# Performance work log

Measured on AMD Instinct MI355X. Metric: run time of the kernel, lower is better.

The kernel has to match this reference:

```python
import jax, jax.numpy as jnp
import numpy as np

DIM = 512
NUM_HEADS = 8
HEAD_DIM = DIM // NUM_HEADS
EPS = 1e-6


def setup_inputs() -> dict:
    key = jax.random.key(0)
    k_x, k_qkv, k_out, k_b = jax.random.split(key, 4)
    B, N = 8, 4096
    x = jax.random.normal(k_x, (B, N, DIM), dtype=jnp.float32)
    # nn.Linear weights stored as [out_features, in_features]; we keep [in, out] for x @ W
    s_qkv = 1.0 / np.sqrt(DIM)
    W_qkv = jax.random.uniform(k_qkv, (DIM, 3 * DIM), minval=-s_qkv, maxval=s_qkv, dtype=jnp.float32)
    W_out = jax.random.uniform(k_out, (DIM, DIM), minval=-s_qkv, maxval=s_qkv, dtype=jnp.float32)
    b_out = jax.random.uniform(k_b, (DIM,), minval=-s_qkv, maxval=s_qkv, dtype=jnp.float32)
    return {"x": x, "W_qkv": W_qkv, "W_out": W_out, "b_out": b_out}


def _feature_map(x):
    # elu(x) + 1
    return jax.nn.elu(x) + 1.0


def reference(x, W_qkv, W_out, b_out):
    B, N, C = x.shape
    H, D = NUM_HEADS, HEAD_DIM
    qkv = x @ W_qkv                              # [B, N, 3C]
    qkv = qkv.reshape(B, N, 3, H, D).transpose(2, 0, 3, 1, 4)  # [3, B, H, N, D]
    q, k, v = qkv[0], qkv[1], qkv[2]
    q_phi = _feature_map(q)                      # [B, H, N, D]
    k_phi = _feature_map(k)
    KV = jnp.einsum('bhnd,bhne->bhde', k_phi, v)  # [B, H, D, D]
    K_sum = k_phi.sum(axis=2)                     # [B, H, D]
    denom = jnp.einsum('bhnd,bhd->bhn', q_phi, K_sum)[..., None] + EPS  # [B, H, N, 1]
    out = jnp.einsum('bhnd,bhde->bhne', q_phi, KV) / denom              # [B, H, N, D]
    out = out.transpose(0, 2, 1, 3).reshape(B, N, C)
    return out @ W_out + b_out
```

## Files before the change

### kernel.cpp

```cpp
#include <hip/hip_runtime.h>
#include <stdint.h>

typedef float    f32x4 __attribute__((ext_vector_type(4)));
typedef short    s16x8 __attribute__((ext_vector_type(8)));
typedef short    s16x4 __attribute__((ext_vector_type(4)));
typedef unsigned short u16;
typedef uint32_t u32;

#define DEVINL __device__ __forceinline__

DEVINL float bf2f(u16 u) { union { u32 i; float f; } x; x.i = ((u32)u) << 16; return x.f; }
DEVINL u16 f2bf(float f) {
  union { float f; u32 i; } x; x.f = f;
  u32 i = x.i;
  return (u16)((i + 0x7FFFu + ((i >> 16) & 1u)) >> 16);
}

DEVINL void gload16(const void* g, void* l) {
  __builtin_amdgcn_global_load_lds((const __attribute__((address_space(1))) void*)g,
                                   (__attribute__((address_space(3))) void*)l,
                                   16, 0, 0);
}

__global__ __launch_bounds__(256) void k_prep(const float* __restrict__ x,
                                              u16* __restrict__ xb,
                                              const float* __restrict__ Wqkv,
                                              u16* __restrict__ wqkvt,
                                              const float* __restrict__ Wout,
                                              u16* __restrict__ woutt) {
  __shared__ __align__(16) float t[64][65];
  int b = blockIdx.x;
  int tid = threadIdx.x;
  if (b < 2048) {
    const int n8 = 2097152;
    int stride = 2048 * 256;
    for (int i = b * 256 + tid; i < n8; i += stride) {
      const f32x4* p = (const f32x4*)(x + (size_t)i * 8);
      f32x4 a = p[0], c = p[1];
      s16x8 o;
      o[0] = (short)f2bf(a[0]); o[1] = (short)f2bf(a[1]);
      o[2] = (short)f2bf(a[2]); o[3] = (short)f2bf(a[3]);
      o[4] = (short)f2bf(c[0]); o[5] = (short)f2bf(c[1]);
      o[6] = (short)f2bf(c[2]); o[7] = (short)f2bf(c[3]);
      *(s16x8*)(xb + (size_t)i * 8) = o;
    }
    return;
  }
  const float* W; u16* Wt; int K, N, tb;
  if (b < 2048 + 192) { W = Wqkv; Wt = wqkvt; K = 512; N = 1536; tb = b - 2048; }
  else               { W = Wout; Wt = woutt; K = 512; N = 512;  tb = b - 2240; }
  int nb = N >> 6;
  int tn = tb % nb, tk = tb / nb;
  int n0 = tn << 6, k0 = tk << 6;
  int cr = tid >> 4, cc = (tid & 15) << 2;
#pragma unroll
  for (int i = 0; i < 4; i++) {
    int r = cr + (i << 4);
    f32x4 v = *(const f32x4*)(W + (size_t)(k0 + r) * N + n0 + cc);
    t[r][cc] = v[0]; t[r][cc + 1] = v[1]; t[r][cc + 2] = v[2]; t[r][cc + 3] = v[3];
  }
  __syncthreads();
#pragma unroll
  for (int i = 0; i < 4; i++) {
    int nn = cr + (i << 4);
    s16x4 o;
    o[0] = (short)f2bf(t[cc    ][nn]);
    o[1] = (short)f2bf(t[cc + 1][nn]);
    o[2] = (short)f2bf(t[cc + 2][nn]);
    o[3] = (short)f2bf(t[cc + 3][nn]);
    *(s16x4*)(Wt + (size_t)(n0 + nn) * K + k0 + cc) = o;
  }
}

template <int EPI>
__global__ __launch_bounds__(512, 1) void k_gemm(
    const u16* __restrict__ A, const u16* __restrict__ Bt,
    int nbn,
    u16* __restrict__ qph, u16* __restrict__ kphT, u16* __restrict__ vT,
    float* __restrict__ out, const float* __restrict__ bias) {
  __shared__ __align__(16) u16 lsA[3][256 * 32];
  __shared__ __align__(16) u16 lsB[3][256 * 32];

  int nwg = gridDim.x;
  int bx = blockIdx.x;
  int o = (bx & 7) * (nwg >> 3) + (bx >> 3);
  int bm = o / nbn, bn = o % nbn;
  int m0 = bm << 8, n0 = bn << 8;
  int tid = threadIdx.x;
  int w = tid >> 6, lane = tid & 63;
  int lnlo = lane & 15, lnhi = lane >> 4;
  int wr = w >> 2, wc = w & 3;

  const u16* gAp[2]; const u16* gBp[2]; int ldst[2];
#pragma unroll
  for (int i = 0; i < 2; i++) {
    int c = tid + i * 512;
    int row = c >> 2, ch = c & 3;
    int gch = ch ^ ((row >> 1) & 3);
    gAp[i] = A + (size_t)(m0 + row) * 512 + gch * 8;
    gBp[i] = Bt + (size_t)(n0 + row) * 512 + gch * 8;
    ldst[i] = c * 8;
  }

  int offA[8], offB[4];
#pragma unroll
  for (int f = 0; f < 8; f++) {
    int r = wr * 128 + f * 16 + lnlo;
    offA[f] = r * 32 + (lnhi ^ ((r >> 1) & 3)) * 8;
  }
#pragma unroll
  for (int f = 0; f < 4; f++) {
    int r = wc * 64 + f * 16 + lnlo;
    offB[f] = r * 32 + (lnhi ^ ((r >> 1) & 3)) * 8;
  }

  f32x4 acc[8][4] = {};

#pragma unroll
  for (int i = 0; i < 2; i++) gload16(gAp[i], &lsA[0][ldst[i]]);
#pragma unroll
  for (int i = 0; i < 2; i++) gload16(gBp[i], &lsB[0][ldst[i]]);
#pragma unroll
  for (int i = 0; i < 2; i++) gload16(gAp[i] + 32, &lsA[1][ldst[i]]);
#pragma unroll
  for (int i = 0; i < 2; i++) gload16(gBp[i] + 32, &lsB[1][ldst[i]]);
  asm volatile("s_waitcnt vmcnt(4)" ::: "memory");
  __builtin_amdgcn_s_barrier();

#pragma unroll
  for (int t = 0; t < 16; t++) {
    int buf = t % 3;
    const u16* La = &lsA[buf][0];
    const u16* Lb = &lsB[buf][0];
    int k2 = (t + 2) * 32;
    int b2 = (t + 2) % 3;

    s16x8 bf[4], af[4];
#pragma unroll
    for (int f = 0; f < 4; f++) bf[f] = *(const s16x8*)(Lb + offB[f]);
#pragma unroll
    for (int f = 0; f < 4; f++) af[f] = *(const s16x8*)(La + offA[f]);
    if (t < 14) {
#pragma unroll
      for (int i = 0; i < 2; i++) gload16(gAp[i] + k2, &lsA[b2][ldst[i]]);
    }
    __builtin_amdgcn_s_barrier();
    __builtin_amdgcn_s_setprio(1);
#pragma unroll
    for (int mf = 0; mf < 4; mf++)
#pragma unroll
      for (int nf = 0; nf < 4; nf++)
        acc[mf][nf] = __builtin_amdgcn_mfma_f32_16x16x32_bf16(af[mf], bf[nf], acc[mf][nf], 0, 0, 0);
    __builtin_amdgcn_s_setprio(0);
    __builtin_amdgcn_s_barrier();

    s16x8 af2[4];
#pragma unroll
    for (int f = 0; f < 4; f++) af2[f] = *(const s16x8*)(La + offA[4 + f]);
    if (t < 14) {
#pragma unroll
      for (int i = 0; i < 2; i++) gload16(gBp[i] + k2, &lsB[b2][ldst[i]]);
    }
    __builtin_amdgcn_s_barrier();
    __builtin_amdgcn_s_setprio(1);
#pragma unroll
    for (int mf = 0; mf < 4; mf++)
#pragma unroll
      for (int nf = 0; nf < 4; nf++)
        acc[4 + mf][nf] = __builtin_amdgcn_mfma_f32_16x16x32_bf16(af2[mf], bf[nf], acc[4 + mf][nf], 0, 0, 0);
    __builtin_amdgcn_s_setprio(0);
    if (t <= 13)      asm volatile("s_waitcnt vmcnt(4)" ::: "memory");
    else if (t == 14) asm volatile("s_waitcnt vmcnt(0)" ::: "memory");
    if (t < 15) __builtin_amdgcn_s_barrier();
  }

  int gmB = m0 + wr * 128;
  int gnB = n0 + wc * 64;
  if (EPI == 0) {
    int sec = n0 >> 9;
    if (sec == 0) {
#pragma unroll
      for (int mf = 0; mf < 8; mf++) {
#pragma unroll
        for (int nf = 0; nf < 4; nf++) {
          int col = gnB + nf * 16 + lnlo;
          int hh = (col >> 6) & 7;
          int dd = col & 63;
#pragma unroll
          for (int r = 0; r < 4; r++) {
            int rowm = gmB + mf * 16 + lnhi * 4 + r;
            float val = acc[mf][nf][r];
            val = (val > 0.f) ? (val + 1.f) : __expf(val);
            int bidx = rowm >> 12, tok = rowm & 4095;
            qph[(((size_t)(bidx * 8 + hh) * 4096 + tok) << 6) + dd] = f2bf(val);
          }
        }
      }
    } else {
      u16* dstT = (sec == 1) ? kphT : vT;
      bool isphi = (sec == 1);
#pragma unroll
      for (int mf = 0; mf < 8; mf++) {
        int rowm = gmB + mf * 16 + lnhi * 4;
        int bidx = rowm >> 12, tok = rowm & 4095;
#pragma unroll
        for (int nf = 0; nf < 4; nf++) {
          int col = gnB + nf * 16 + lnlo;
          int hh = (col >> 6) & 7;
          int dd = col & 63;
          s16x4 o4;
#pragma unroll
          for (int r = 0; r < 4; r++) {
            float val = acc[mf][nf][r];
            if (isphi) val = (val > 0.f) ? (val + 1.f) : __expf(val);
            o4[r] = (short)f2bf(val);
          }
          *(s16x4*)&dstT[((size_t)(bidx * 8 + hh) * 64 + dd) * 4096 + tok] = o4;
        }
      }
    }
  } else {
#pragma unroll
    for (int mf = 0; mf < 8; mf++) {
#pragma unroll
      for (int nf = 0; nf < 4; nf++) {
        int col = gnB + nf * 16 + lnlo;
        float bv = bias[col];
#pragma unroll
        for (int r = 0; r < 4; r++) {
          int rowm = gmB + mf * 16 + lnhi * 4 + r;
          out[(size_t)rowm * 512 + col] = acc[mf][nf][r] + bv;
        }
      }
    }
  }
}

__global__ __launch_bounds__(256, 2) void k_kv(const u16* __restrict__ kphT,
                                               const u16* __restrict__ vT,
                                               float* __restrict__ kvpart,
                                               float* __restrict__ kspart) {
  __shared__ __align__(16) u16 lsK[64 * 256];
  __shared__ __align__(16) u16 lsV[64 * 256];
  __shared__ float red[4][64];
  int bx = blockIdx.x;
  int bh = bx >> 4, ck = bx & 15;
  int tid = threadIdx.x, w = tid >> 6, lane = tid & 63;
  int lnlo = lane & 15, lnhi = lane >> 4;
  size_t gbase = (size_t)bh * 64 * 4096 + ck * 256;

#pragma unroll
  for (int i = 0; i < 8; i++) {
    int c = tid + i * 256;
    int row = c >> 5, ch = c & 31;
    int gch = ch ^ (row & 31);
    gload16(kphT + gbase + (size_t)row * 4096 + gch * 8, &lsK[c * 8]);
  }
#pragma unroll
  for (int i = 0; i < 8; i++) {
    int c = tid + i * 256;
    int row = c >> 5, ch = c & 31;
    int gch = ch ^ (row & 31);
    gload16(vT + gbase + (size_t)row * 4096 + gch * 8, &lsV[c * 8]);
  }
  asm volatile("s_waitcnt vmcnt(0)" ::: "memory");
  __builtin_amdgcn_s_barrier();

  f32x4 acc[4] = {{0.f, 0.f, 0.f, 0.f}, {0.f, 0.f, 0.f, 0.f},
                  {0.f, 0.f, 0.f, 0.f}, {0.f, 0.f, 0.f, 0.f}};
  int rb = w * 16 + lnlo;
#pragma unroll
  for (int kk = 0; kk < 8; kk++) {
    s16x8 bfr = *(const s16x8*)&lsV[rb * 256 + ((kk * 4 + lnhi) ^ (rb & 31)) * 8];
#pragma unroll
    for (int mf = 0; mf < 4; mf++) {
      int ra = mf * 16 + lnlo;
      s16x8 af = *(const s16x8*)&lsK[ra * 256 + ((kk * 4 + lnhi) ^ (ra & 31)) * 8];
      acc[mf] = __builtin_amdgcn_mfma_f32_16x16x32_bf16(af, bfr, acc[mf], 0, 0, 0);
    }
  }

  {
    int d = tid & 63, q = tid >> 6;
    float s = 0.f;
#pragma unroll
    for (int j = 0; j < 8; j++) {
      s16x8 v8 = *(const s16x8*)&lsK[d * 256 + (q * 8 + j) * 8];
#pragma unroll
      for (int e = 0; e < 8; e++) s += bf2f((u16)v8[e]);
    }
    red[q][d] = s;
  }
  __syncthreads();

  size_t pb = (size_t)(bh * 16 + ck) * 4096;
#pragma unroll
  for (int mf = 0; mf < 4; mf++)
#pragma unroll
    for (int r = 0; r < 4; r++)
      kvpart[pb + (size_t)(mf * 16 + lnhi * 4 + r) * 64 + (w * 16 + lnlo)] = acc[mf][r];
  if (tid < 64)
    kspart[(size_t)(bh * 16 + ck) * 64 + tid] =
        red[0][tid] + red[1][tid] + red[2][tid] + red[3][tid];
}

__global__ __launch_bounds__(256) void k_kvred(const float* __restrict__ kvpart,
                                               const float* __restrict__ kspart,
                                               u16* __restrict__ kvt_sw,
                                               float* __restrict__ ksum) {
  int bh = blockIdx.x;
  int tid = threadIdx.x;
  int e = tid >> 2, d0 = (tid & 3) * 16;
  size_t pb = (size_t)bh * 16 * 4096;
#pragma unroll
  for (int dd = 0; dd < 16; dd++) {
    int d = d0 + dd;
    float s = 0.f;
#pragma unroll
    for (int c = 0; c < 16; c++) s += kvpart[pb + (size_t)c * 4096 + d * 64 + e];
    int chs = (d >> 3) ^ (e & 7);
    kvt_sw[((size_t)bh * 64 + e) * 64 + chs * 8 + (d & 7)] = f2bf(s);
  }
  if (tid < 64) {
    float s = 0.f;
#pragma unroll
    for (int c = 0; c < 16; c++) s += kspart[(size_t)bh * 1024 + c * 64 + tid];
    ksum[bh * 64 + tid] = s;
  }
}

__global__ __launch_bounds__(256, 2) void k_attnout(const u16* __restrict__ qphi,
                                                    const u16* __restrict__ kvt_sw,
                                                    const float* __restrict__ ksum,
                                                    u16* __restrict__ y) {
  __shared__ __align__(16) u16 qa[256 * 64];
  __shared__ __align__(16) u16 bb[64 * 64];
  __shared__ float ksl[64];
  __shared__ float rdnl[256];
  int bx = blockIdx.x;
  int bh = bx >> 4, tch = bx & 15;
  int b = bh >> 3, hh = bh & 7;
  int tid = threadIdx.x, w = tid >> 6, lane = tid & 63;
  int lnlo = lane & 15, lnhi = lane >> 4;
  size_t qbase = ((size_t)bh * 4096 + tch * 256) * 64;

#pragma unroll
  for (int i = 0; i < 8; i++) {
    int c = i * 256 + tid;
    int row = c >> 3, ch = c & 7;
    int gcol = (ch ^ (row & 7)) << 3;
    gload16(qphi + qbase + (size_t)row * 64 + gcol, &qa[c * 8]);
  }
#pragma unroll
  for (int i = 0; i < 2; i++) {
    int c = i * 256 + tid;
    gload16(kvt_sw + (size_t)bh * 4096 + c * 8, &bb[c * 8]);
  }
  if (tid < 64) ksl[tid] = ksum[bh * 64 + tid];
  __syncthreads();

  {
    float den = 0.f;
#pragma unroll
    for (int ch = 0; ch < 8; ch++) {
      s16x8 v8 = *(const s16x8*)&qa[tid * 64 + ((ch ^ (tid & 7)) << 3)];
#pragma unroll
      for (int j = 0; j < 8; j++) den += bf2f((u16)v8[j]) * ksl[ch * 8 + j];
    }
    rdnl[tid] = 1.f / (den + 1e-6f);
  }
  __syncthreads();

  f32x4 acc[4][4] = {};
#pragma unroll
  for (int kk = 0; kk < 2; kk++) {
    s16x8 af[4], bfr[4];
#pragma unroll
    for (int f = 0; f < 4; f++) {
      int ra = w * 64 + f * 16 + lnlo;
      int ca = (kk * 4 + lnhi) ^ (ra & 7);
      af[f] = *(const s16x8*)&qa[ra * 64 + ca * 8];
      int rb = f * 16 + lnlo;
      int cb = (kk * 4 + lnhi) ^ (rb & 7);
      bfr[f] = *(const s16x8*)&bb[rb * 64 + cb * 8];
    }
#pragma unroll
    for (int mf = 0; mf < 4; mf++)
#pragma unroll
      for (int nf = 0; nf < 4; nf++)
        acc[mf][nf] = __builtin_amdgcn_mfma_f32_16x16x32_bf16(af[mf], bfr[nf], acc[mf][nf], 0, 0, 0);
  }

  size_t yrow0 = (size_t)b * 4096 + tch * 256;
#pragma unroll
  for (int mf = 0; mf < 4; mf++) {
#pragma unroll
    for (int nf = 0; nf < 4; nf++) {
      int e = nf * 16 + lnlo;
#pragma unroll
      for (int r = 0; r < 4; r++) {
        int tl = w * 64 + mf * 16 + lnhi * 4 + r;
        float val = acc[mf][nf][r] * rdnl[tl];
        y[(yrow0 + tl) * 512 + hh * 64 + e] = f2bf(val);
      }
    }
  }
}

#define OFF_XB     ((size_t)0)
#define OFF_WQKVT  ((size_t)33554432)
#define OFF_WOUTT  ((size_t)35127296)
#define OFF_QPHI   ((size_t)35651584)
#define OFF_KPHI   ((size_t)69206016)
#define OFF_VBUF   ((size_t)102760448)
#define OFF_KVPART ((size_t)136314880)
#define OFF_KSPART ((size_t)153092096)
#define OFF_KVT    ((size_t)153354240)
#define OFF_KSUM   ((size_t)153878528)

extern "C" void kernel_launch(void* const* d_in, const int* in_sizes, int n_in,
                              void* d_out, int out_size, void* d_ws, size_t ws_size,
                              hipStream_t stream) {
  const float* x    = (const float*)d_in[0];
  const float* Wqkv = (const float*)d_in[1];
  const float* Wout = (const float*)d_in[2];
  const float* bout = (const float*)d_in[3];
  float* out = (float*)d_out;
  char* ws = (char*)d_ws;

  u16* xb     = (u16*)(ws + OFF_XB);
  u16* y      = (u16*)(ws + OFF_XB);
  u16* wqkvt  = (u16*)(ws + OFF_WQKVT);
  u16* woutt  = (u16*)(ws + OFF_WOUTT);
  u16* qphi   = (u16*)(ws + OFF_QPHI);
  u16* kphT   = (u16*)(ws + OFF_KPHI);
  u16* vT     = (u16*)(ws + OFF_VBUF);
  float* kvpart = (float*)(ws + OFF_KVPART);
  float* kspart = (float*)(ws + OFF_KSPART);
  u16* kvt_sw = (u16*)(ws + OFF_KVT);
  float* ksum = (float*)(ws + OFF_KSUM);

  k_prep<<<2304, 256, 0, stream>>>(x, xb, Wqkv, wqkvt, Wout, woutt);

  k_gemm<0><<<768, 512, 0, stream>>>(xb, wqkvt, 6, qphi, kphT, vT, nullptr, nullptr);
  k_kv<<<64 * 16, 256, 0, stream>>>(kphT, vT, kvpart, kspart);
  k_kvred<<<64, 256, 0, stream>>>(kvpart, kspart, kvt_sw, ksum);
  k_attnout<<<64 * 16, 256, 0, stream>>>(qphi, kvt_sw, ksum, y);
  k_gemm<1><<<256, 512, 0, stream>>>(y, woutt, 2, nullptr, nullptr, nullptr, out, bout);
}
```

Measured before the change: 159.3 us.

## Restructure GEMM main loop to double-buffered 64-wide K tiles with split half-tile loads

The GEMM mainloop moves from a triple-buffered 32-wide K tile to a double-buffered 64-wide K tile. Each operand buffer is split into two 128-row halves that are refilled at a finer grain, interleaved between MFMA groups, with an 8-way XOR swizzle on LDS. The goal is fewer barrier and loop iterations per K, and global-to-LDS loads that overlap more evenly with MFMA work. In exchange it adds many more barriers per tile and a hand-tuned vmcnt schedule that must match the issue order exactly.

```diff
diff --git a/kernel.cpp b/kernel.cpp
--- a/kernel.cpp
+++ b/kernel.cpp
@@ -8,6 +8,7 @@
 typedef uint32_t u32;
 
 #define DEVINL __device__ __forceinline__
+#define BARF do { asm volatile("" ::: "memory"); __builtin_amdgcn_s_barrier(); asm volatile("" ::: "memory"); } while (0)
 
 DEVINL float bf2f(u16 u) { union { u32 i; float f; } x; x.i = ((u32)u) << 16; return x.f; }
 DEVINL u16 f2bf(float f) {
@@ -74,104 +75,119 @@
 
 template <int EPI>
 __global__ __launch_bounds__(512, 1) void k_gemm(
-    const u16* __restrict__ A, const u16* __restrict__ Bt,
-    int nbn,
+    const u16* __restrict__ A, const u16* __restrict__ Bt, int nbn,
     u16* __restrict__ qph, u16* __restrict__ kphT, u16* __restrict__ vT,
     float* __restrict__ out, const float* __restrict__ bias) {
-  __shared__ __align__(16) u16 lsA[3][256 * 32];
-  __shared__ __align__(16) u16 lsB[3][256 * 32];
-
-  int nwg = gridDim.x;
-  int bx = blockIdx.x;
+  __shared__ __align__(16) u16 lsA[2][2][128 * 64];
+  __shared__ __align__(16) u16 lsB[2][2][128 * 64];
+
+  int nwg = gridDim.x, bx = blockIdx.x;
   int o = (bx & 7) * (nwg >> 3) + (bx >> 3);
   int bm = o / nbn, bn = o % nbn;
   int m0 = bm << 8, n0 = bn << 8;
-  int tid = threadIdx.x;
-  int w = tid >> 6, lane = tid & 63;
+  int tid = threadIdx.x, w = tid >> 6, lane = tid & 63;
   int lnlo = lane & 15, lnhi = lane >> 4;
   int wr = w >> 2, wc = w & 3;
 
-  const u16* gAp[2]; const u16* gBp[2]; int ldst[2];
-#pragma unroll
-  for (int i = 0; i < 2; i++) {
-    int c = tid + i * 512;
-    int row = c >> 2, ch = c & 3;
-    int gch = ch ^ ((row >> 1) & 3);
-    gAp[i] = A + (size_t)(m0 + row) * 512 + gch * 8;
-    gBp[i] = Bt + (size_t)(n0 + row) * 512 + gch * 8;
-    ldst[i] = c * 8;
-  }
-
-  int offA[8], offB[4];
-#pragma unroll
-  for (int f = 0; f < 8; f++) {
-    int r = wr * 128 + f * 16 + lnlo;
-    offA[f] = r * 32 + (lnhi ^ ((r >> 1) & 3)) * 8;
-  }
-#pragma unroll
-  for (int f = 0; f < 4; f++) {
-    int r = wc * 64 + f * 16 + lnlo;
-    offB[f] = r * 32 + (lnhi ^ ((r >> 1) & 3)) * 8;
-  }
+  int c0 = tid, c1 = tid + 512;
+  int r0 = c0 >> 3, r1 = c1 >> 3;
+  int g0 = ((c0 & 7) ^ (r0 & 7)) * 8, g1 = ((c1 & 7) ^ (r1 & 7)) * 8;
+  const u16* gA[2][2]; const u16* gB[2][2];
+#pragma unroll
+  for (int h = 0; h < 2; h++) {
+    gA[h][0] = A + (size_t)(m0 + h * 128 + r0) * 512 + g0;
+    gA[h][1] = A + (size_t)(m0 + h * 128 + r1) * 512 + g1;
+    gB[h][0] = Bt + (size_t)(n0 + h * 128 + r0) * 512 + g0;
+    gB[h][1] = Bt + (size_t)(n0 + h * 128 + r1) * 512 + g1;
+  }
+  int l0 = c0 * 8, l1 = c1 * 8;
+
+  auto SA = [&](int buf, int h, int kt) {
+    gload16(gA[h][0] + kt * 64, &lsA[buf][h][l0]);
+    gload16(gA[h][1] + kt * 64, &lsA[buf][h][l1]);
+  };
+  auto SB = [&](int buf, int h, int kt) {
+    gload16(gB[h][0] + kt * 64, &lsB[buf][h][l0]);
+    gload16(gB[h][1] + kt * 64, &lsB[buf][h][l1]);
+  };
+
+  int offA[2][8], offB[2][4];
+#pragma unroll
+  for (int kk = 0; kk < 2; kk++) {
+#pragma unroll
+    for (int mf = 0; mf < 8; mf++) {
+      int r = mf * 16 + lnlo;
+      offA[kk][mf] = r * 64 + (((kk * 4 + lnhi) ^ (r & 7))) * 8;
+    }
+#pragma unroll
+    for (int nf = 0; nf < 4; nf++) {
+      int r = (wc & 1) * 64 + nf * 16 + lnlo;
+      offB[kk][nf] = r * 64 + (((kk * 4 + lnhi) ^ (r & 7))) * 8;
+    }
+  }
+  const u16* LA0 = &lsA[0][wr][0];
+  const u16* LA1 = &lsA[1][wr][0];
+  const u16* LB0 = &lsB[0][wc >> 1][0];
+  const u16* LB1 = &lsB[1][wc >> 1][0];
 
   f32x4 acc[8][4] = {};
-
-#pragma unroll
-  for (int i = 0; i < 2; i++) gload16(gAp[i], &lsA[0][ldst[i]]);
-#pragma unroll
-  for (int i = 0; i < 2; i++) gload16(gBp[i], &lsB[0][ldst[i]]);
-#pragma unroll
-  for (int i = 0; i < 2; i++) gload16(gAp[i] + 32, &lsA[1][ldst[i]]);
-#pragma unroll
-  for (int i = 0; i < 2; i++) gload16(gBp[i] + 32, &lsB[1][ldst[i]]);
-  asm volatile("s_waitcnt vmcnt(4)" ::: "memory");
-  __builtin_amdgcn_s_barrier();
-
-#pragma unroll
-  for (int t = 0; t < 16; t++) {
-    int buf = t % 3;
-    const u16* La = &lsA[buf][0];
-    const u16* Lb = &lsB[buf][0];
-    int k2 = (t + 2) * 32;
-    int b2 = (t + 2) % 3;
-
-    s16x8 bf[4], af[4];
-#pragma unroll
-    for (int f = 0; f < 4; f++) bf[f] = *(const s16x8*)(Lb + offB[f]);
-#pragma unroll
-    for (int f = 0; f < 4; f++) af[f] = *(const s16x8*)(La + offA[f]);
-    if (t < 14) {
-#pragma unroll
-      for (int i = 0; i < 2; i++) gload16(gAp[i] + k2, &lsA[b2][ldst[i]]);
-    }
-    __builtin_amdgcn_s_barrier();
+  s16x8 af[4], bf[4];
+
+  auto rdA = [&](const u16* base, int kk, int g) {
+#pragma unroll
+    for (int f = 0; f < 4; f++) af[f] = *(const s16x8*)(base + offA[kk][g * 4 + f]);
+  };
+  auto rdB = [&](const u16* base, int kk) {
+#pragma unroll
+    for (int f = 0; f < 4; f++) bf[f] = *(const s16x8*)(base + offB[kk][f]);
+  };
+  auto MG = [&](int g) {
     __builtin_amdgcn_s_setprio(1);
 #pragma unroll
     for (int mf = 0; mf < 4; mf++)
 #pragma unroll
       for (int nf = 0; nf < 4; nf++)
-        acc[mf][nf] = __builtin_amdgcn_mfma_f32_16x16x32_bf16(af[mf], bf[nf], acc[mf][nf], 0, 0, 0);
+        acc[g * 4 + mf][nf] =
+            __builtin_amdgcn_mfma_f32_16x16x32_bf16(af[mf], bf[nf], acc[g * 4 + mf][nf], 0, 0, 0);
     __builtin_amdgcn_s_setprio(0);
-    __builtin_amdgcn_s_barrier();
-
-    s16x8 af2[4];
-#pragma unroll
-    for (int f = 0; f < 4; f++) af2[f] = *(const s16x8*)(La + offA[4 + f]);
-    if (t < 14) {
-#pragma unroll
-      for (int i = 0; i < 2; i++) gload16(gBp[i] + k2, &lsB[b2][ldst[i]]);
-    }
-    __builtin_amdgcn_s_barrier();
-    __builtin_amdgcn_s_setprio(1);
-#pragma unroll
-    for (int mf = 0; mf < 4; mf++)
-#pragma unroll
-      for (int nf = 0; nf < 4; nf++)
-        acc[4 + mf][nf] = __builtin_amdgcn_mfma_f32_16x16x32_bf16(af2[mf], bf[nf], acc[4 + mf][nf], 0, 0, 0);
-    __builtin_amdgcn_s_setprio(0);
-    if (t <= 13)      asm volatile("s_waitcnt vmcnt(4)" ::: "memory");
-    else if (t == 14) asm volatile("s_waitcnt vmcnt(0)" ::: "memory");
-    if (t < 15) __builtin_amdgcn_s_barrier();
+  };
+
+  SB(0, 0, 0); SB(0, 1, 0); SA(0, 0, 0); SA(0, 1, 0); SB(1, 0, 1);
+  asm volatile("s_waitcnt vmcnt(2)" ::: "memory");
+  BARF;
+
+#pragma unroll
+  for (int j = 0; j < 4; j++) {
+    const int tb = 2 * j + 1, tn0 = 2 * j + 2, tn1 = 2 * j + 3;
+    const bool st = (j < 3);
+    rdB(LB0, 0); rdA(LA0, 0, 0); SB(1, 1, tb);
+    BARF; MG(0); BARF;
+    rdA(LA0, 0, 1); SA(1, 0, tb);
+    BARF; MG(1); BARF;
+    rdB(LB0, 1); rdA(LA0, 1, 0); SA(1, 1, tb);
+    BARF; MG(0); BARF;
+    rdA(LA0, 1, 1);
+    if (st) SB(0, 0, tn0);
+    BARF; MG(1);
+    if (st) asm volatile("s_waitcnt vmcnt(2)" ::: "memory");
+    else    asm volatile("s_waitcnt vmcnt(0)" ::: "memory");
+    BARF;
+    rdB(LB1, 0); rdA(LA1, 0, 0);
+    if (st) SB(0, 1, tn0);
+    BARF; MG(0); BARF;
+    rdA(LA1, 0, 1);
+    if (st) SA(0, 0, tn0);
+    BARF; MG(1); BARF;
+    rdB(LB1, 1); rdA(LA1, 1, 0);
+    if (st) SA(0, 1, tn0);
+    BARF; MG(0); BARF;
+    rdA(LA1, 1, 1);
+    if (st) SB(1, 0, tn1);
+    BARF; MG(1);
+    if (st) {
+      asm volatile("s_waitcnt vmcnt(2)" ::: "memory");
+      BARF;
+    }
   }
 
   int gmB = m0 + wr * 128;
```

Measured after the change: 155.7 us. 1.02x faster.
